# Kernel tuning notes

Measured on AMD Instinct MI355X. Metric: run time of the kernel, lower is better.

The kernel has to match this reference:

```python
import jax, jax.numpy as jnp
import numpy as np

# e2m1 FP4 value table: sign bit in nibble MSB, values {0,0.5,1,1.5,2,3,4,6}
_E2M1 = jnp.array([0.0, 0.5, 1.0, 1.5, 2.0, 3.0, 4.0, 6.0,
                   -0.0, -0.5, -1.0, -1.5, -2.0, -3.0, -4.0, -6.0], dtype=jnp.float32)


def _dequant_fp4(packed, scales, group_size):
    """packed: [E, out, in//8] uint32; scales: [E, in//group_size, out] -> [E, out, in] f32."""
    shifts = jnp.arange(8, dtype=jnp.uint32) * 4  # nibble shift amounts 0,4,...,28
    nib = (packed[..., None] >> shifts) & jnp.uint32(0xF)  # [E, out, in//8, 8]
    E, O, P, _ = nib.shape
    nib = nib.reshape(E, O, P * 8).astype(jnp.int32)
    w = _E2M1[nib]  # [E, out, in] f32
    gids = jnp.arange(P * 8) // group_size  # group id per input column
    sc = jnp.transpose(scales, (0, 2, 1))[:, :, gids]  # [E, out, in]
    return w * sc


def setup_inputs() -> dict:
    E, H, I, T, K, G = 8, 2048, 1408, 2048, 2, 128
    key = jax.random.key(0)
    ks = jax.random.split(key, 9)
    x = jax.random.normal(ks[0], (T, H), dtype=jnp.float32)
    gate_packed = jax.random.bits(ks[1], (E, I, H // 8), dtype=jnp.uint32)
    up_packed = jax.random.bits(ks[2], (E, I, H // 8), dtype=jnp.uint32)
    down_packed = jax.random.bits(ks[3], (E, H, I // 8), dtype=jnp.uint32)
    gate_scales = jax.random.uniform(ks[4], (E, H // G, I), jnp.float32, 0.5, 1.5)
    up_scales = jax.random.uniform(ks[5], (E, H // G, I), jnp.float32, 0.5, 1.5)
    down_scales = jax.random.uniform(ks[6], (E, I // G, H), jnp.float32, 0.5, 1.5)
    topk_idx = jax.random.randint(ks[7], (T, K), 0, E, dtype=jnp.int32)
    w = jax.random.uniform(ks[8], (T, K), jnp.float32)
    topk_w = w / jnp.sum(w, axis=-1, keepdims=True)
    return {"x": x,
            "gate_packed": gate_packed, "gate_scales": gate_scales,
            "up_packed": up_packed, "up_scales": up_scales,
            "down_packed": down_packed, "down_scales": down_scales,
            "topk_idx": topk_idx, "topk_w": topk_w, "group_size": G}


def reference(x, gate_packed, gate_scales, up_packed, up_scales,
              down_packed, down_scales, topk_idx, topk_w, group_size):
    # Fused dequant (nibble unpack + e2m1 table + per-group scale) for all experts
    gate_w = _dequant_fp4(gate_packed, gate_scales, group_size)  # [E, I, H]
    up_w = _dequant_fp4(up_packed, up_scales, group_size)        # [E, I, H]
    down_w = _dequant_fp4(down_packed, down_scales, group_size)  # [E, H, I]
    # Grouped SwiGLU expert MLP (dense over E=8 experts, gather routed outputs)
    g = jnp.einsum('th,eih->eti', x, gate_w)
    u = jnp.einsum('th,eih->eti', x, up_w)
    h = jax.nn.silu(g) * u                                        # [E, T, I]
    y = jnp.einsum('eti,ehi->eth', h, down_w)                     # [E, T, H]
    T = x.shape[0]
    sel = y[topk_idx, jnp.arange(T)[:, None], :]                  # [T, K, H]
    return jnp.sum(sel * topk_w[..., None], axis=1)               # [T, H]
```

## Files before the change

kernel.cpp:

```cpp
#include <hip/hip_runtime.h>
#include <hip/hip_bf16.h>
#include <stdint.h>

#define E_ 8
#define H_ 2048
#define I_ 1408
#define T_ 2048
#define K_ 2
#define G_ 128

typedef __bf16 bf16;
typedef bf16 bf16x8 __attribute__((ext_vector_type(8)));
typedef float f32x4 __attribute__((ext_vector_type(4)));

__device__ __forceinline__ uint32_t prm(uint32_t hi, uint32_t lo, uint32_t sel) {
    return __builtin_amdgcn_perm(hi, lo, sel);
}

struct DequantTab { uint32_t thi0, thi1, tlo0, tlo1; };

__device__ __forceinline__ DequantTab build_tab(float s) {
    union { bf16 h[8]; uint32_t u[4]; } tb;
    tb.h[0] = (bf16)(0.0f);
    tb.h[1] = (bf16)(0.5f * s);
    tb.h[2] = (bf16)(1.0f * s);
    tb.h[3] = (bf16)(1.5f * s);
    tb.h[4] = (bf16)(2.0f * s);
    tb.h[5] = (bf16)(3.0f * s);
    tb.h[6] = (bf16)(4.0f * s);
    tb.h[7] = (bf16)(6.0f * s);
    DequantTab t;
    t.thi0 = prm(tb.u[1], tb.u[0], 0x07050301u);
    t.tlo0 = prm(tb.u[1], tb.u[0], 0x06040200u);
    t.thi1 = prm(tb.u[3], tb.u[2], 0x07050301u);
    t.tlo1 = prm(tb.u[3], tb.u[2], 0x06040200u);
    return t;
}

__device__ __forceinline__ uint4 dequant8t(uint32_t p, const DequantTab& t) {
    const uint32_t pr = p >> 4;
    const uint32_t pe = p  & 0x07070707u;
    const uint32_t po = pr & 0x07070707u;
    const uint32_t He = prm(t.thi1, t.thi0, pe) | ((p  & 0x08080808u) << 4);
    const uint32_t Le = prm(t.tlo1, t.tlo0, pe);
    const uint32_t Ho = prm(t.thi1, t.thi0, po) | ((pr & 0x08080808u) << 4);
    const uint32_t Lo = prm(t.tlo1, t.tlo0, po);
    const uint32_t E01 = prm(He, Le, 0x05010400u);
    const uint32_t E23 = prm(He, Le, 0x07030602u);
    const uint32_t O01 = prm(Ho, Lo, 0x05010400u);
    const uint32_t O23 = prm(Ho, Lo, 0x07030602u);
    return make_uint4(prm(O01, E01, 0x05040100u),
                      prm(O01, E01, 0x07060302u),
                      prm(O23, E23, 0x05040100u),
                      prm(O23, E23, 0x07060302u));
}

__device__ __forceinline__ void gld16(void* lds, const void* g) {
    __builtin_amdgcn_global_load_lds(
        (__attribute__((address_space(1))) void*)g,
        (__attribute__((address_space(3))) void*)lds, 16, 0, 0);
}

__global__ void route_count(const int* __restrict__ topk_idx, int* __restrict__ counts) {
    int p = blockIdx.x * blockDim.x + threadIdx.x;
    if (p < T_ * K_) atomicAdd(&counts[topk_idx[p]], 1);
}

__global__ void route_scan(const int* __restrict__ counts, int* __restrict__ offsets,
                           int* __restrict__ tmap) {
    if (threadIdx.x == 0) {
        int acc = 0, ti = 0;
        for (int e = 0; e < E_; e++) {
            offsets[e] = acc;
            int nt = (counts[e] + 63) >> 6;
            for (int j = 0; j < nt; j++) tmap[ti++] = (e << 16) | j;
            acc += counts[e];
        }
        offsets[E_] = acc;
        for (; ti < 128; ti++) tmap[ti] = -1;
    }
}

__global__ void route_fill(const int* __restrict__ topk_idx, const float* __restrict__ topk_w,
                           int* __restrict__ cursors, const int* __restrict__ offsets,
                           int* __restrict__ tok, float* __restrict__ wgt,
                           int* __restrict__ inv) {
    int p = blockIdx.x * blockDim.x + threadIdx.x;
    if (p < T_ * K_) {
        int e = topk_idx[p];
        int slot = atomicAdd(&cursors[e], 1);
        int idx = offsets[e] + slot;
        tok[idx] = p / K_;
        wgt[idx] = topk_w[p];
        inv[p] = idx;
    }
}

__global__ __launch_bounds__(256)
void xcast_kernel(const float* __restrict__ x, uint4* __restrict__ xb) {
    const int i = blockIdx.x * 256 + threadIdx.x;
    const float4 a = ((const float4*)x)[i * 2];
    const float4 b = ((const float4*)x)[i * 2 + 1];
    union { uint4 u; bf16 h[8]; } r;
    r.h[0] = (bf16)a.x; r.h[1] = (bf16)a.y; r.h[2] = (bf16)a.z; r.h[3] = (bf16)a.w;
    r.h[4] = (bf16)b.x; r.h[5] = (bf16)b.y; r.h[6] = (bf16)b.z; r.h[7] = (bf16)b.w;
    xb[i] = r.u;
}

__global__ __launch_bounds__(256, 4)
void gemm1t_kernel(const bf16* __restrict__ xb,
                   const uint32_t* __restrict__ gate_packed,
                   const float* __restrict__ gate_scales,
                   const uint32_t* __restrict__ up_packed,
                   const float* __restrict__ up_scales,
                   const int* __restrict__ offsets,
                   const int* __restrict__ tmap,
                   const int* __restrict__ tok, bf16* __restrict__ h_buf)
{
    const int tm = tmap[blockIdx.x];
    if (tm < 0) return;
    const int e = tm >> 16, ty = tm & 0xffff;
    const int row0 = offsets[e];
    const int cnt = offsets[e + 1] - row0;
    const int itile = blockIdx.y;

    __shared__ __align__(16) bf16 xs[64][64];
    __shared__ __align__(16) bf16 wgs[64][64];
    __shared__ __align__(16) bf16 wus[64][64];

    const int tid = threadIdx.x;

    const int xr0 = tid >> 3;
    const int xr1 = xr0 + 32;
    const int xc  = tid & 7;
    int g0 = ty * 64 + xr0;  g0 = (g0 < cnt) ? g0 : (cnt - 1);
    int g1 = ty * 64 + xr1;  g1 = (g1 < cnt) ? g1 : (cnt - 1);
    const bf16* xsrc0 = xb + (size_t)tok[row0 + g0] * H_ + ((xc ^ (xr0 & 7)) * 8);
    const bf16* xsrc1 = xb + (size_t)tok[row0 + g1] * H_ + ((xc ^ (xr1 & 7)) * 8);
    bf16* xdst0 = &xs[xr0][xc * 8];
    bf16* xdst1 = &xs[xr1][xc * 8];

    const int mat  = tid >> 7;
    const int id   = tid & 127;
    const int wrow = id >> 1;
    const int quad = id & 1;
    const int irow = itile * 64 + wrow;
    const uint32_t* wp_row = (mat ? up_packed : gate_packed)
        + (size_t)e * I_ * (H_ / 8) + (size_t)irow * (H_ / 8) + quad * 4;
    const float* ws_row = (mat ? up_scales : gate_scales)
        + (size_t)e * (H_ / G_) * I_ + irow;
    bf16 (* const wdst)[64] = mat ? wus : wgs;

    const int wave = tid >> 6, lane = tid & 63;
    const int wy = wave >> 1, wx = wave & 1;
    const int lrow = lane & 15, kq = lane >> 4;

    f32x4 accg[2][2] = {};
    f32x4 accu[2][2] = {};

    for (int kg = 0; kg < H_ / G_; kg++) {
        const DequantTab tw = build_tab(ws_row[kg * I_]);
#pragma unroll
        for (int kh2 = 0; kh2 < 2; kh2++) {
            const int k0 = kg * 128 + kh2 * 64;
            gld16(xdst0, xsrc0 + k0);
            gld16(xdst1, xsrc1 + k0);
            const uint4 pw = *(const uint4*)(wp_row + (k0 >> 3));
            {
                uint4 d0 = dequant8t(pw.x, tw);
                uint4 d1 = dequant8t(pw.y, tw);
                uint4 d2 = dequant8t(pw.z, tw);
                uint4 d3 = dequant8t(pw.w, tw);
                const int cb = quad * 4, rs = wrow & 7;
                *(uint4*)&wdst[wrow][((cb + 0) ^ rs) * 8] = d0;
                *(uint4*)&wdst[wrow][((cb + 1) ^ rs) * 8] = d1;
                *(uint4*)&wdst[wrow][((cb + 2) ^ rs) * 8] = d2;
                *(uint4*)&wdst[wrow][((cb + 3) ^ rs) * 8] = d3;
            }
            __syncthreads();

#pragma unroll
            for (int kh = 0; kh < 2; kh++) {
                bf16x8 a[2], bg[2], bu[2];
#pragma unroll
                for (int mi = 0; mi < 2; mi++) {
                    const int ra = wy * 32 + mi * 16 + lrow;
                    a[mi] = *(const bf16x8*)&xs[ra][((kh * 4 + kq) ^ (ra & 7)) * 8];
                }
#pragma unroll
                for (int ni = 0; ni < 2; ni++) {
                    const int rb = wx * 32 + ni * 16 + lrow;
                    const int cb = ((kh * 4 + kq) ^ (rb & 7)) * 8;
                    bg[ni] = *(const bf16x8*)&wgs[rb][cb];
                    bu[ni] = *(const bf16x8*)&wus[rb][cb];
                }
#pragma unroll
                for (int mi = 0; mi < 2; mi++)
#pragma unroll
                    for (int ni = 0; ni < 2; ni++) {
                        accg[mi][ni] = __builtin_amdgcn_mfma_f32_16x16x32_bf16(a[mi], bg[ni], accg[mi][ni], 0, 0, 0);
                        accu[mi][ni] = __builtin_amdgcn_mfma_f32_16x16x32_bf16(a[mi], bu[ni], accu[mi][ni], 0, 0, 0);
                    }
            }
            __syncthreads();
        }
    }

#pragma unroll
    for (int mi = 0; mi < 2; mi++)
#pragma unroll
        for (int ni = 0; ni < 2; ni++) {
            const int icol = itile * 64 + wx * 32 + ni * 16 + lrow;
#pragma unroll
            for (int r = 0; r < 4; r++) {
                const int grow = ty * 64 + wy * 32 + mi * 16 + kq * 4 + r;
                if (grow < cnt) {
                    const float gv = accg[mi][ni][r];
                    const float hv = gv / (1.f + __expf(-gv)) * accu[mi][ni][r];
                    h_buf[(size_t)(row0 + grow) * I_ + icol] = (bf16)hv;
                }
            }
        }
}

__global__ __launch_bounds__(256, 4)
void gemm2t_kernel(const bf16* __restrict__ h_buf,
                   const uint32_t* __restrict__ down_packed,
                   const float* __restrict__ down_scales,
                   const int* __restrict__ offsets,
                   const int* __restrict__ tmap,
                   const float* __restrict__ wgt, float* __restrict__ yp)
{
    const int tm = tmap[blockIdx.x];
    if (tm < 0) return;
    const int e = tm >> 16, ty = tm & 0xffff;
    const int row0 = offsets[e];
    const int cnt = offsets[e + 1] - row0;
    const int htile = blockIdx.y;

    __shared__ __align__(16) bf16 hs[64][64];
    __shared__ __align__(16) bf16 wds[128][64];

    const int tid = threadIdx.x;

    const int xr0 = tid >> 3;
    const int xr1 = xr0 + 32;
    const int xc  = tid & 7;
    int g0 = ty * 64 + xr0;  g0 = (g0 < cnt) ? g0 : (cnt - 1);
    int g1 = ty * 64 + xr1;  g1 = (g1 < cnt) ? g1 : (cnt - 1);
    const bf16* hsrc0 = h_buf + (size_t)(row0 + g0) * I_ + ((xc ^ (xr0 & 7)) * 8);
    const bf16* hsrc1 = h_buf + (size_t)(row0 + g1) * I_ + ((xc ^ (xr1 & 7)) * 8);
    bf16* hdst0 = &hs[xr0][xc * 8];
    bf16* hdst1 = &hs[xr1][xc * 8];

    const int wrow = tid >> 1;
    const int quad = tid & 1;
    const int hrow = htile * 128 + wrow;
    const uint32_t* dp_row = down_packed + (size_t)e * H_ * (I_ / 8) + (size_t)hrow * (I_ / 8) + quad * 4;
    const float* ds_row = down_scales + (size_t)e * (I_ / G_) * H_ + hrow;

    const int wave = tid >> 6, lane = tid & 63;
    const int wy = wave >> 1, wx = wave & 1;
    const int lrow = lane & 15, kq = lane >> 4;

    f32x4 acc[2][4] = {};

    for (int kg = 0; kg < I_ / G_; kg++) {
        const DequantTab td = build_tab(ds_row[kg * H_]);
#pragma unroll
        for (int kh2 = 0; kh2 < 2; kh2++) {
            const int k0 = kg * 128 + kh2 * 64;
            gld16(hdst0, hsrc0 + k0);
            gld16(hdst1, hsrc1 + k0);
            const uint4 pw = *(const uint4*)(dp_row + (k0 >> 3));
            {
                uint4 d0 = dequant8t(pw.x, td);
                uint4 d1 = dequant8t(pw.y, td);
                uint4 d2 = dequant8t(pw.z, td);
                uint4 d3 = dequant8t(pw.w, td);
                const int cb = quad * 4, rs = wrow & 7;
                *(uint4*)&wds[wrow][((cb + 0) ^ rs) * 8] = d0;
                *(uint4*)&wds[wrow][((cb + 1) ^ rs) * 8] = d1;
                *(uint4*)&wds[wrow][((cb + 2) ^ rs) * 8] = d2;
                *(uint4*)&wds[wrow][((cb + 3) ^ rs) * 8] = d3;
            }
            __syncthreads();

#pragma unroll
            for (int kh = 0; kh < 2; kh++) {
                bf16x8 a[2], b[4];
#pragma unroll
                for (int mi = 0; mi < 2; mi++) {
                    const int ra = wy * 32 + mi * 16 + lrow;
                    a[mi] = *(const bf16x8*)&hs[ra][((kh * 4 + kq) ^ (ra & 7)) * 8];
                }
#pragma unroll
                for (int ni = 0; ni < 4; ni++) {
                    const int rb = wx * 64 + ni * 16 + lrow;
                    b[ni] = *(const bf16x8*)&wds[rb][((kh * 4 + kq) ^ (rb & 7)) * 8];
                }
#pragma unroll
                for (int mi = 0; mi < 2; mi++)
#pragma unroll
                    for (int ni = 0; ni < 4; ni++)
                        acc[mi][ni] = __builtin_amdgcn_mfma_f32_16x16x32_bf16(a[mi], b[ni], acc[mi][ni], 0, 0, 0);
            }
            __syncthreads();
        }
    }

#pragma unroll
    for (int mi = 0; mi < 2; mi++)
#pragma unroll
        for (int r = 0; r < 4; r++) {
            const int lr = wy * 32 + mi * 16 + kq * 4 + r;
            const int grow = ty * 64 + lr;
            if (grow < cnt) {
                const float w = wgt[row0 + grow];
#pragma unroll
                for (int ni = 0; ni < 4; ni++) {
                    const int col = htile * 128 + wx * 64 + ni * 16 + lrow;
                    yp[(size_t)(row0 + grow) * H_ + col] = acc[mi][ni][r] * w;
                }
            }
        }
}

__global__ __launch_bounds__(256)
void combine_kernel(const float* __restrict__ yp, const int* __restrict__ inv,
                    float* __restrict__ out) {
    const int idx = blockIdx.x * 256 + threadIdx.x;
    const int t = idx >> 9;
    const int c = idx & 511;
    const float4 a = ((const float4*)yp)[(size_t)inv[t * 2] * (H_ / 4) + c];
    const float4 b = ((const float4*)yp)[(size_t)inv[t * 2 + 1] * (H_ / 4) + c];
    float4 o;
    o.x = a.x + b.x; o.y = a.y + b.y; o.z = a.z + b.z; o.w = a.w + b.w;
    ((float4*)out)[idx] = o;
}

extern "C" void kernel_launch(void* const* d_in, const int* in_sizes, int n_in,
                              void* d_out, int out_size, void* d_ws, size_t ws_size,
                              hipStream_t stream) {
    const float* x = (const float*)d_in[0];
    const uint32_t* gate_packed = (const uint32_t*)d_in[1];
    const float* gate_scales = (const float*)d_in[2];
    const uint32_t* up_packed = (const uint32_t*)d_in[3];
    const float* up_scales = (const float*)d_in[4];
    const uint32_t* down_packed = (const uint32_t*)d_in[5];
    const float* down_scales = (const float*)d_in[6];
    const int* topk_idx = (const int*)d_in[7];
    const float* topk_w = (const float*)d_in[8];
    float* out = (float*)d_out;

    char* ws = (char*)d_ws;
    int* counts  = (int*)ws;
    int* cursors = (int*)(ws + 32);
    int* offsets = (int*)(ws + 64);
    int* tmap    = (int*)(ws + 128);
    int* tok     = (int*)(ws + 640);
    float* wgt   = (float*)(ws + 17024);
    int* inv     = (int*)(ws + 33408);
    bf16* h_buf  = (bf16*)(ws + 49792);
    bf16* xb     = (bf16*)(ws + 49792 + 11534336ull);
    float* yp    = (float*)(ws + 49792 + 11534336ull + 8388608ull);

    hipMemsetAsync(d_ws, 0, 1024, stream);

    route_count<<<(T_ * K_ + 255) / 256, 256, 0, stream>>>(topk_idx, counts);
    route_scan<<<1, 64, 0, stream>>>(counts, offsets, tmap);
    route_fill<<<(T_ * K_ + 255) / 256, 256, 0, stream>>>(topk_idx, topk_w, cursors, offsets,
                                                          tok, wgt, inv);
    xcast_kernel<<<T_ * H_ / 8 / 256, 256, 0, stream>>>(x, (uint4*)xb);

    dim3 g1(72, I_ / 64);
    gemm1t_kernel<<<g1, 256, 0, stream>>>(xb, gate_packed, gate_scales, up_packed, up_scales,
                                          offsets, tmap, tok, h_buf);
    dim3 g2(72, H_ / 128);
    gemm2t_kernel<<<g2, 256, 0, stream>>>(h_buf, down_packed, down_scales,
                                          offsets, tmap, wgt, yp);
    combine_kernel<<<T_ * H_ / 4 / 256, 256, 0, stream>>>(yp, inv, out);
}
```

Baseline: 288.2 us.

## Double M tile to 128 tokens and double-buffer activation loads in both GEMMs

Both expert GEMMs now process 128 routed tokens per block instead of 64, so each dequantized weight tile is reused across twice as many rows and the redundant FP4 dequant work drops by roughly half. Activation tiles are double-buffered in LDS, with the next slice's async global-to-LDS loads and packed-weight fetch issued before the current MFMA work, and dequant of the next weight slice placed after compute. Token indices are staged in shared memory once per block. The cost is more LDS and accumulator registers (launch bounds lowered to 3 blocks per SM), fewer blocks launched, and more padding waste on partial expert tiles.

```diff
diff --git a/kernel.cpp b/kernel.cpp
--- a/kernel.cpp
+++ b/kernel.cpp
@@ -72,12 +72,12 @@
         int acc = 0, ti = 0;
         for (int e = 0; e < E_; e++) {
             offsets[e] = acc;
-            int nt = (counts[e] + 63) >> 6;
+            int nt = (counts[e] + 127) >> 7;
             for (int j = 0; j < nt; j++) tmap[ti++] = (e << 16) | j;
             acc += counts[e];
         }
         offsets[E_] = acc;
-        for (; ti < 128; ti++) tmap[ti] = -1;
+        for (; ti < 64; ti++) tmap[ti] = -1;
     }
 }
 
@@ -107,8 +107,8 @@
     xb[i] = r.u;
 }
 
-__global__ __launch_bounds__(256, 4)
-void gemm1t_kernel(const bf16* __restrict__ xb,
+__global__ __launch_bounds__(256, 3)
+void gemm1q_kernel(const bf16* __restrict__ xb,
                    const uint32_t* __restrict__ gate_packed,
                    const float* __restrict__ gate_scales,
                    const uint32_t* __restrict__ up_packed,
@@ -124,96 +124,116 @@
     const int cnt = offsets[e + 1] - row0;
     const int itile = blockIdx.y;
 
-    __shared__ __align__(16) bf16 xs[64][64];
+    __shared__ __align__(16) bf16 xs[2][128][64];
     __shared__ __align__(16) bf16 wgs[64][64];
     __shared__ __align__(16) bf16 wus[64][64];
+    __shared__ int toks[128];
 
     const int tid = threadIdx.x;
-
-    const int xr0 = tid >> 3;
-    const int xr1 = xr0 + 32;
-    const int xc  = tid & 7;
-    int g0 = ty * 64 + xr0;  g0 = (g0 < cnt) ? g0 : (cnt - 1);
-    int g1 = ty * 64 + xr1;  g1 = (g1 < cnt) ? g1 : (cnt - 1);
-    const bf16* xsrc0 = xb + (size_t)tok[row0 + g0] * H_ + ((xc ^ (xr0 & 7)) * 8);
-    const bf16* xsrc1 = xb + (size_t)tok[row0 + g1] * H_ + ((xc ^ (xr1 & 7)) * 8);
-    bf16* xdst0 = &xs[xr0][xc * 8];
-    bf16* xdst1 = &xs[xr1][xc * 8];
+    if (tid < 128) {
+        int r = ty * 128 + tid;
+        toks[tid] = tok[row0 + ((r < cnt) ? r : (cnt - 1))];
+    }
+    __syncthreads();
+
+    const bf16* xsrc[4];
+    int xf[4];
+#pragma unroll
+    for (int i = 0; i < 4; i++) {
+        const int f = i * 256 + tid;
+        const int r = f >> 3, c = f & 7;
+        xf[i] = f;
+        xsrc[i] = xb + (size_t)toks[r] * H_ + ((c ^ (r & 7)) * 8);
+    }
 
     const int mat  = tid >> 7;
     const int id   = tid & 127;
     const int wrow = id >> 1;
     const int quad = id & 1;
     const int irow = itile * 64 + wrow;
-    const uint32_t* wp_row = (mat ? up_packed : gate_packed)
+    const uint32_t* wp = (mat ? up_packed : gate_packed)
         + (size_t)e * I_ * (H_ / 8) + (size_t)irow * (H_ / 8) + quad * 4;
     const float* ws_row = (mat ? up_scales : gate_scales)
         + (size_t)e * (H_ / G_) * I_ + irow;
     bf16 (* const wdst)[64] = mat ? wus : wgs;
+    const int cb = quad * 4, rs = wrow & 7;
 
     const int wave = tid >> 6, lane = tid & 63;
     const int wy = wave >> 1, wx = wave & 1;
     const int lrow = lane & 15, kq = lane >> 4;
 
-    f32x4 accg[2][2] = {};
-    f32x4 accu[2][2] = {};
-
-    for (int kg = 0; kg < H_ / G_; kg++) {
-        const DequantTab tw = build_tab(ws_row[kg * I_]);
-#pragma unroll
-        for (int kh2 = 0; kh2 < 2; kh2++) {
-            const int k0 = kg * 128 + kh2 * 64;
-            gld16(xdst0, xsrc0 + k0);
-            gld16(xdst1, xsrc1 + k0);
-            const uint4 pw = *(const uint4*)(wp_row + (k0 >> 3));
-            {
-                uint4 d0 = dequant8t(pw.x, tw);
-                uint4 d1 = dequant8t(pw.y, tw);
-                uint4 d2 = dequant8t(pw.z, tw);
-                uint4 d3 = dequant8t(pw.w, tw);
-                const int cb = quad * 4, rs = wrow & 7;
-                *(uint4*)&wdst[wrow][((cb + 0) ^ rs) * 8] = d0;
-                *(uint4*)&wdst[wrow][((cb + 1) ^ rs) * 8] = d1;
-                *(uint4*)&wdst[wrow][((cb + 2) ^ rs) * 8] = d2;
-                *(uint4*)&wdst[wrow][((cb + 3) ^ rs) * 8] = d3;
-            }
+    f32x4 accg[4][2] = {};
+    f32x4 accu[4][2] = {};
+
+    uint4 pw = *(const uint4*)wp;
+    DequantTab tw = build_tab(ws_row[0]);
+#pragma unroll
+    for (int i = 0; i < 4; i++)
+        gld16((char*)&xs[0][0][0] + xf[i] * 16, xsrc[i]);
+    {
+        uint4 d0 = dequant8t(pw.x, tw), d1 = dequant8t(pw.y, tw);
+        uint4 d2 = dequant8t(pw.z, tw), d3 = dequant8t(pw.w, tw);
+        *(uint4*)&wdst[wrow][((cb + 0) ^ rs) * 8] = d0;
+        *(uint4*)&wdst[wrow][((cb + 1) ^ rs) * 8] = d1;
+        *(uint4*)&wdst[wrow][((cb + 2) ^ rs) * 8] = d2;
+        *(uint4*)&wdst[wrow][((cb + 3) ^ rs) * 8] = d3;
+    }
+    __syncthreads();
+
+    for (int ks = 0; ks < 32; ks++) {
+        const int b = ks & 1;
+        const bool hasn = (ks < 31);
+        uint4 pw_n;
+        if (hasn) {
+            pw_n = *(const uint4*)(wp + (ks + 1) * 8);
+#pragma unroll
+            for (int i = 0; i < 4; i++)
+                gld16((char*)&xs[b ^ 1][0][0] + xf[i] * 16, xsrc[i] + (ks + 1) * 64);
+        }
+#pragma unroll
+        for (int kh = 0; kh < 2; kh++) {
+            bf16x8 a[4], bg[2], bu[2];
+#pragma unroll
+            for (int mi = 0; mi < 4; mi++) {
+                const int ra = wy * 64 + mi * 16 + lrow;
+                a[mi] = *(const bf16x8*)&xs[b][ra][((kh * 4 + kq) ^ (ra & 7)) * 8];
+            }
+#pragma unroll
+            for (int ni = 0; ni < 2; ni++) {
+                const int rb = wx * 32 + ni * 16 + lrow;
+                const int cc = ((kh * 4 + kq) ^ (rb & 7)) * 8;
+                bg[ni] = *(const bf16x8*)&wgs[rb][cc];
+                bu[ni] = *(const bf16x8*)&wus[rb][cc];
+            }
+#pragma unroll
+            for (int mi = 0; mi < 4; mi++)
+#pragma unroll
+                for (int ni = 0; ni < 2; ni++) {
+                    accg[mi][ni] = __builtin_amdgcn_mfma_f32_16x16x32_bf16(a[mi], bg[ni], accg[mi][ni], 0, 0, 0);
+                    accu[mi][ni] = __builtin_amdgcn_mfma_f32_16x16x32_bf16(a[mi], bu[ni], accu[mi][ni], 0, 0, 0);
+                }
+        }
+        __syncthreads();
+        if (hasn) {
+            if (ks & 1) tw = build_tab(ws_row[((ks + 1) >> 1) * I_]);
+            uint4 d0 = dequant8t(pw_n.x, tw), d1 = dequant8t(pw_n.y, tw);
+            uint4 d2 = dequant8t(pw_n.z, tw), d3 = dequant8t(pw_n.w, tw);
+            *(uint4*)&wdst[wrow][((cb + 0) ^ rs) * 8] = d0;
+            *(uint4*)&wdst[wrow][((cb + 1) ^ rs) * 8] = d1;
+            *(uint4*)&wdst[wrow][((cb + 2) ^ rs) * 8] = d2;
+            *(uint4*)&wdst[wrow][((cb + 3) ^ rs) * 8] = d3;
             __syncthreads();
-
-#pragma unroll
-            for (int kh = 0; kh < 2; kh++) {
-                bf16x8 a[2], bg[2], bu[2];
-#pragma unroll
-                for (int mi = 0; mi < 2; mi++) {
-                    const int ra = wy * 32 + mi * 16 + lrow;
-                    a[mi] = *(const bf16x8*)&xs[ra][((kh * 4 + kq) ^ (ra & 7)) * 8];
-                }
-#pragma unroll
-                for (int ni = 0; ni < 2; ni++) {
-                    const int rb = wx * 32 + ni * 16 + lrow;
-                    const int cb = ((kh * 4 + kq) ^ (rb & 7)) * 8;
-                    bg[ni] = *(const bf16x8*)&wgs[rb][cb];
-                    bu[ni] = *(const bf16x8*)&wus[rb][cb];
-                }
-#pragma unroll
-                for (int mi = 0; mi < 2; mi++)
-#pragma unroll
-                    for (int ni = 0; ni < 2; ni++) {
-                        accg[mi][ni] = __builtin_amdgcn_mfma_f32_16x16x32_bf16(a[mi], bg[ni], accg[mi][ni], 0, 0, 0);
-                        accu[mi][ni] = __builtin_amdgcn_mfma_f32_16x16x32_bf16(a[mi], bu[ni], accu[mi][ni], 0, 0, 0);
-                    }
-            }
-            __syncthreads();
-        }
-    }
-
-#pragma unroll
-    for (int mi = 0; mi < 2; mi++)
+        }
+    }
+
+#pragma unroll
+    for (int mi = 0; mi < 4; mi++)
 #pragma unroll
         for (int ni = 0; ni < 2; ni++) {
             const int icol = itile * 64 + wx * 32 + ni * 16 + lrow;
 #pragma unroll
             for (int r = 0; r < 4; r++) {
-                const int grow = ty * 64 + wy * 32 + mi * 16 + kq * 4 + r;
+                const int grow = ty * 128 + wy * 64 + mi * 16 + kq * 4 + r;
                 if (grow < cnt) {
                     const float gv = accg[mi][ni][r];
                     const float hv = gv / (1.f + __expf(-gv)) * accu[mi][ni][r];
@@ -223,8 +243,8 @@
         }
 }
 
-__global__ __launch_bounds__(256, 4)
-void gemm2t_kernel(const bf16* __restrict__ h_buf,
+__global__ __launch_bounds__(256, 3)
+void gemm2q_kernel(const bf16* __restrict__ h_buf,
                    const uint32_t* __restrict__ down_packed,
                    const float* __restrict__ down_scales,
                    const int* __restrict__ offsets,
@@ -238,83 +258,97 @@
     const int cnt = offsets[e + 1] - row0;
     const int htile = blockIdx.y;
 
-    __shared__ __align__(16) bf16 hs[64][64];
+    __shared__ __align__(16) bf16 hs[2][128][64];
     __shared__ __align__(16) bf16 wds[128][64];
 
     const int tid = threadIdx.x;
 
-    const int xr0 = tid >> 3;
-    const int xr1 = xr0 + 32;
-    const int xc  = tid & 7;
-    int g0 = ty * 64 + xr0;  g0 = (g0 < cnt) ? g0 : (cnt - 1);
-    int g1 = ty * 64 + xr1;  g1 = (g1 < cnt) ? g1 : (cnt - 1);
-    const bf16* hsrc0 = h_buf + (size_t)(row0 + g0) * I_ + ((xc ^ (xr0 & 7)) * 8);
-    const bf16* hsrc1 = h_buf + (size_t)(row0 + g1) * I_ + ((xc ^ (xr1 & 7)) * 8);
-    bf16* hdst0 = &hs[xr0][xc * 8];
-    bf16* hdst1 = &hs[xr1][xc * 8];
+    const bf16* hsrc[4];
+    int hf[4];
+#pragma unroll
+    for (int i = 0; i < 4; i++) {
+        const int f = i * 256 + tid;
+        const int r = f >> 3, c = f & 7;
+        int g = ty * 128 + r;  g = (g < cnt) ? g : (cnt - 1);
+        hf[i] = f;
+        hsrc[i] = h_buf + (size_t)(row0 + g) * I_ + ((c ^ (r & 7)) * 8);
+    }
 
     const int wrow = tid >> 1;
     const int quad = tid & 1;
     const int hrow = htile * 128 + wrow;
-    const uint32_t* dp_row = down_packed + (size_t)e * H_ * (I_ / 8) + (size_t)hrow * (I_ / 8) + quad * 4;
+    const uint32_t* dp = down_packed + (size_t)e * H_ * (I_ / 8) + (size_t)hrow * (I_ / 8) + quad * 4;
     const float* ds_row = down_scales + (size_t)e * (I_ / G_) * H_ + hrow;
+    const int cb = quad * 4, rs = wrow & 7;
 
     const int wave = tid >> 6, lane = tid & 63;
     const int wy = wave >> 1, wx = wave & 1;
     const int lrow = lane & 15, kq = lane >> 4;
 
-    f32x4 acc[2][4] = {};
-
-    for (int kg = 0; kg < I_ / G_; kg++) {
-        const DequantTab td = build_tab(ds_row[kg * H_]);
-#pragma unroll
-        for (int kh2 = 0; kh2 < 2; kh2++) {
-            const int k0 = kg * 128 + kh2 * 64;
-            gld16(hdst0, hsrc0 + k0);
-            gld16(hdst1, hsrc1 + k0);
-            const uint4 pw = *(const uint4*)(dp_row + (k0 >> 3));
-            {
-                uint4 d0 = dequant8t(pw.x, td);
-                uint4 d1 = dequant8t(pw.y, td);
-                uint4 d2 = dequant8t(pw.z, td);
-                uint4 d3 = dequant8t(pw.w, td);
-                const int cb = quad * 4, rs = wrow & 7;
-                *(uint4*)&wds[wrow][((cb + 0) ^ rs) * 8] = d0;
-                *(uint4*)&wds[wrow][((cb + 1) ^ rs) * 8] = d1;
-                *(uint4*)&wds[wrow][((cb + 2) ^ rs) * 8] = d2;
-                *(uint4*)&wds[wrow][((cb + 3) ^ rs) * 8] = d3;
-            }
+    f32x4 acc[4][4] = {};
+
+    uint4 pw = *(const uint4*)dp;
+    DequantTab tw = build_tab(ds_row[0]);
+#pragma unroll
+    for (int i = 0; i < 4; i++)
+        gld16((char*)&hs[0][0][0] + hf[i] * 16, hsrc[i]);
+    {
+        uint4 d0 = dequant8t(pw.x, tw), d1 = dequant8t(pw.y, tw);
+        uint4 d2 = dequant8t(pw.z, tw), d3 = dequant8t(pw.w, tw);
+        *(uint4*)&wds[wrow][((cb + 0) ^ rs) * 8] = d0;
+        *(uint4*)&wds[wrow][((cb + 1) ^ rs) * 8] = d1;
+        *(uint4*)&wds[wrow][((cb + 2) ^ rs) * 8] = d2;
+        *(uint4*)&wds[wrow][((cb + 3) ^ rs) * 8] = d3;
+    }
+    __syncthreads();
+
+    for (int ks = 0; ks < I_ / 64; ks++) {
+        const int b = ks & 1;
+        const bool hasn = (ks < I_ / 64 - 1);
+        uint4 pw_n;
+        if (hasn) {
+            pw_n = *(const uint4*)(dp + (ks + 1) * 8);
+#pragma unroll
+            for (int i = 0; i < 4; i++)
+                gld16((char*)&hs[b ^ 1][0][0] + hf[i] * 16, hsrc[i] + (ks + 1) * 64);
+        }
+#pragma unroll
+        for (int kh = 0; kh < 2; kh++) {
+            bf16x8 a[4], bb[4];
+#pragma unroll
+            for (int mi = 0; mi < 4; mi++) {
+                const int ra = wy * 64 + mi * 16 + lrow;
+                a[mi] = *(const bf16x8*)&hs[b][ra][((kh * 4 + kq) ^ (ra & 7)) * 8];
+            }
+#pragma unroll
+            for (int ni = 0; ni < 4; ni++) {
+                const int rb = wx * 64 + ni * 16 + lrow;
+                bb[ni] = *(const bf16x8*)&wds[rb][((kh * 4 + kq) ^ (rb & 7)) * 8];
+            }
+#pragma unroll
+            for (int mi = 0; mi < 4; mi++)
+#pragma unroll
+                for (int ni = 0; ni < 4; ni++)
+                    acc[mi][ni] = __builtin_amdgcn_mfma_f32_16x16x32_bf16(a[mi], bb[ni], acc[mi][ni], 0, 0, 0);
+        }
+        __syncthreads();
+        if (hasn) {
+            if (ks & 1) tw = build_tab(ds_row[((ks + 1) >> 1) * H_]);
+            uint4 d0 = dequant8t(pw_n.x, tw), d1 = dequant8t(pw_n.y, tw);
+            uint4 d2 = dequant8t(pw_n.z, tw), d3 = dequant8t(pw_n.w, tw);
+            *(uint4*)&wds[wrow][((cb + 0) ^ rs) * 8] = d0;
+            *(uint4*)&wds[wrow][((cb + 1) ^ rs) * 8] = d1;
+            *(uint4*)&wds[wrow][((cb + 2) ^ rs) * 8] = d2;
+            *(uint4*)&wds[wrow][((cb + 3) ^ rs) * 8] = d3;
             __syncthreads();
-
-#pragma unroll
-            for (int kh = 0; kh < 2; kh++) {
-                bf16x8 a[2], b[4];
-#pragma unroll
-                for (int mi = 0; mi < 2; mi++) {
-                    const int ra = wy * 32 + mi * 16 + lrow;
-                    a[mi] = *(const bf16x8*)&hs[ra][((kh * 4 + kq) ^ (ra & 7)) * 8];
-                }
-#pragma unroll
-                for (int ni = 0; ni < 4; ni++) {
-                    const int rb = wx * 64 + ni * 16 + lrow;
-                    b[ni] = *(const bf16x8*)&wds[rb][((kh * 4 + kq) ^ (rb & 7)) * 8];
-                }
-#pragma unroll
-                for (int mi = 0; mi < 2; mi++)
-#pragma unroll
-                    for (int ni = 0; ni < 4; ni++)
-                        acc[mi][ni] = __builtin_amdgcn_mfma_f32_16x16x32_bf16(a[mi], b[ni], acc[mi][ni], 0, 0, 0);
-            }
-            __syncthreads();
-        }
-    }
-
-#pragma unroll
-    for (int mi = 0; mi < 2; mi++)
+        }
+    }
+
+#pragma unroll
+    for (int mi = 0; mi < 4; mi++)
 #pragma unroll
         for (int r = 0; r < 4; r++) {
-            const int lr = wy * 32 + mi * 16 + kq * 4 + r;
-            const int grow = ty * 64 + lr;
+            const int grow = ty * 128 + wy * 64 + mi * 16 + kq * 4 + r;
             if (grow < cnt) {
                 const float w = wgt[row0 + grow];
 #pragma unroll
@@ -373,11 +407,11 @@
                                                           tok, wgt, inv);
     xcast_kernel<<<T_ * H_ / 8 / 256, 256, 0, stream>>>(x, (uint4*)xb);
 
-    dim3 g1(72, I_ / 64);
-    gemm1t_kernel<<<g1, 256, 0, stream>>>(xb, gate_packed, gate_scales, up_packed, up_scales,
+    dim3 g1(40, I_ / 64);
+    gemm1q_kernel<<<g1, 256, 0, stream>>>(xb, gate_packed, gate_scales, up_packed, up_scales,
                                           offsets, tmap, tok, h_buf);
-    dim3 g2(72, H_ / 128);
-    gemm2t_kernel<<<g2, 256, 0, stream>>>(h_buf, down_packed, down_scales,
+    dim3 g2(40, H_ / 128);
+    gemm2q_kernel<<<g2, 256, 0, stream>>>(h_buf, down_packed, down_scales,
                                           offsets, tmap, wgt, yp);
     combine_kernel<<<T_ * H_ / 4 / 256, 256, 0, stream>>>(yp, inv, out);
 }
```

Result: no change. 291.8 us (+1.2%).
